# Kernel tuning notes

Hardware: AMD Instinct MI355X
Metric: run time of the kernel (lower is better)

Reference implementation:

```python
import math
import jax, jax.numpy as jnp
import numpy as np

D, H, NB, L, K = 45, 256, 6, 2, 8          # features, hidden, maf blocks, made hidden layers, spline bins
M = 3 * K - 1                               # params per feature (tails='linear')
TAIL = -math.log(1e-6)                      # tail_bound = -log(alpha)
MIN_BW = MIN_BH = MIN_D = 1e-3


def _masks():
    # nflows MADE sequential degrees (random_mask=False)
    d_in = np.arange(1, D + 1)
    d_h = (np.arange(H) % (D - 1)) + 1
    m0 = (d_h[:, None] >= d_in[None, :]).astype(np.float32)   # [H, D]
    mh = (d_h[:, None] >= d_h[None, :]).astype(np.float32)    # [H, H]
    d_out = np.repeat(d_in, M)                                 # nflows tile(): each degree repeated M times
    mf = (d_out[:, None] > d_h[None, :]).astype(np.float32)   # [D*M, H], strict for output layer
    return jnp.asarray(m0), jnp.asarray(mh), jnp.asarray(mf)


def _rq_spline(x, params):
    # x: [B, D]; params: [B, D, M]. unconstrained_rational_quadratic_spline, tails='linear'.
    uw = params[..., :K] / math.sqrt(H)        # nflows divides by sqrt(hidden_features)
    uh = params[..., K:2 * K] / math.sqrt(H)
    const = math.log(math.exp(1.0 - MIN_D) - 1.0)
    ud = jnp.pad(params[..., 2 * K:], ((0, 0), (0, 0), (1, 1)), constant_values=const)  # [B,D,K+1]
    inside = (x >= -TAIL) & (x <= TAIL)
    xc = jnp.clip(x, -TAIL, TAIL)

    def bin_edges(u, mn):
        p = jax.nn.softmax(u, -1)
        p = mn + (1.0 - mn * K) * p
        c = jnp.pad(jnp.cumsum(p, -1), ((0, 0), (0, 0), (1, 0)))
        c = 2.0 * TAIL * c - TAIL
        c = c.at[..., 0].set(-TAIL).at[..., -1].set(TAIL)
        return c, c[..., 1:] - c[..., :-1]

    cw, w = bin_edges(uw, MIN_BW)              # cumwidths [B,D,K+1], widths [B,D,K]
    ch, h = bin_edges(uh, MIN_BH)
    d = MIN_D + jax.nn.softplus(ud)            # derivatives [B,D,K+1]

    idx = jnp.clip(jnp.sum((xc[..., None] >= cw), -1) - 1, 0, K - 1)[..., None]
    g = lambda a: jnp.take_along_axis(a, idx, -1)[..., 0]
    icw, ibw, ich, ih = g(cw[..., :-1]), g(w), g(ch[..., :-1]), g(h)
    idelta = g(h / w)
    id0, id1 = g(d[..., :-1]), g(d[..., 1:])

    th = (xc - icw) / ibw
    th1 = th * (1.0 - th)
    den = idelta + (id0 + id1 - 2.0 * idelta) * th1
    y = ich + ih * (idelta * th * th + id0 * th1) / den
    lad = jnp.log(idelta * idelta * (id1 * th * th + 2.0 * idelta * th1 + id0 * (1.0 - th) ** 2)) - 2.0 * jnp.log(den)
    return jnp.where(inside, y, x), jnp.where(inside, lad, 0.0)


def setup_inputs() -> dict:
    key = jax.random.key(0)
    ks = jax.random.split(key, 10)
    B, s = 32768, 0.02
    return {
        "x": jax.random.normal(ks[0], (B, D), jnp.float32),
        "cond": jax.random.normal(ks[1], (B, 1), jnp.float32),
        "W0": jax.random.normal(ks[2], (NB, H, D), jnp.float32) * s,
        "b0": jax.random.normal(ks[3], (NB, H), jnp.float32) * s,
        "Wc": jax.random.normal(ks[4], (NB, H, 1), jnp.float32) * s,
        "bc": jax.random.normal(ks[5], (NB, H), jnp.float32) * s,
        "Wh": jax.random.normal(ks[6], (NB, L, H, H), jnp.float32) * s,
        "bh": jax.random.normal(ks[7], (NB, L, H), jnp.float32) * s,
        "Wf": jax.random.normal(ks[8], (NB, D * M, H), jnp.float32) * s,
        "bf": jax.random.normal(ks[9], (NB, D * M), jnp.float32) * s,
    }


def reference(x, cond, W0, b0, Wc, bc, Wh, bh, Wf, bf):
    m0, mh, mf = _masks()
    z = x
    ld = jnp.zeros(x.shape[0], x.dtype)
    for b in range(NB):  # CompositeTransform of NB MAF blocks
        hid = z @ (W0[b] * m0).T + b0[b] + cond @ Wc[b].T + bc[b]
        for l in range(L):  # MaskedFeedforwardBlock: linear -> ReLU (dropout=0, no BN)
            hid = jax.nn.relu(hid @ (Wh[b, l] * mh).T + bh[b, l])
        params = (hid @ (Wf[b] * mf).T + bf[b]).reshape(z.shape[0], D, M)
        z, lad = _rq_spline(z, params)
        ld = ld + lad.sum(-1)
    log_z = 0.5 * D * math.log(2.0 * math.pi)
    return -0.5 * jnp.sum(z * z, axis=1) - log_z + ld
```

## Files before the change

kernel.cpp:

```cpp
#include <hip/hip_runtime.h>


typedef __bf16 bf16;
typedef __bf16 bf16x8 __attribute__((ext_vector_type(8)));
typedef float  f32x16 __attribute__((ext_vector_type(16)));

#define TAILF  13.815510557964274f
#define TAIL2  27.631021115928548f
#define CMIN   0.027631021115928548f
#define LOGZ   41.352233994210265f

#define WS_W0M   0
#define WS_WHM   196608
#define WS_WFM   1769472
#define WS_BEFF  5210112
#define WS_BFP   5216256
#define WS_WCC   5243136
#define WS_BHP   5249280
#define WS_NEED  5261568

#define N_W0  (6*256*64)
#define N_WH  (6*2*256*256)
#define N_WF  (6*5*224*256)
#define N_PREP (N_W0 + N_WH + N_WF)

__device__ __forceinline__ int s_deg(int s) {
    return (s < 216) ? (s / 6) : (36 + (s - 216) / 5);
}
__device__ __forceinline__ int s_orig(int s) {
    int d, rk;
    if (s < 216) { d = s / 6; rk = s - d * 6; }
    else { int u = s - 216; d = 36 + u / 5; rk = u - (u / 5) * 5; }
    return d + 44 * rk;
}

__global__ void prep_all(const float* __restrict__ W0, const float* __restrict__ b0,
                         const float* __restrict__ Wc, const float* __restrict__ bc,
                         const float* __restrict__ Wh, const float* __restrict__ Wf,
                         const float* __restrict__ bfv, const float* __restrict__ bh,
                         bf16* __restrict__ W0m, bf16* __restrict__ Whm,
                         bf16* __restrict__ Wfm,
                         float* __restrict__ beff, float* __restrict__ bfp,
                         float* __restrict__ Wcc, float* __restrict__ bhp)
{
    int idx = blockIdx.x * 256 + threadIdx.x;
    if (idx < N_W0) {
        int j = idx & 7, lane = (idx >> 3) & 63, chunk = idx >> 9;
        int kt = chunk & 3, cg = (chunk >> 2) & 7, b = chunk >> 5;
        int col = cg * 32 + (lane & 31);
        int k   = kt * 16 + (lane >> 5) * 8 + j;
        int o   = s_orig(col);
        float v = 0.f;
        if (k < 45 && s_deg(col) >= k)
            v = W0[(b * 256 + o) * 45 + k];
        W0m[idx] = (bf16)v;
        if (k == 0) {
            beff[b * 256 + col] = b0[b * 256 + o] + bc[b * 256 + o];
            Wcc[b * 256 + col]  = Wc[b * 256 + o];
        }
    } else if (idx < N_W0 + N_WH) {
        int id = idx - N_W0;
        int j = id & 7, lane = (id >> 3) & 63, chunk = id >> 9;
        int kt = chunk & 15, cg = (chunk >> 4) & 7, bl = chunk >> 7;
        int col = cg * 32 + (lane & 31);
        int k   = kt * 16 + (lane >> 5) * 8 + j;
        int oc  = s_orig(col), ok = s_orig(k);
        float v = (s_deg(col) >= s_deg(k)) ? Wh[bl * 65536 + oc * 256 + ok] : 0.f;
        Whm[id] = (bf16)v;
        if (k == 0)
            bhp[bl * 256 + col] = bh[bl * 256 + oc];
    } else if (idx < N_PREP) {
        int id = idx - (N_W0 + N_WH);
        int j = id & 7, lane = (id >> 3) & 63, chunk = id >> 9;
        int kt = chunk & 15, t2 = chunk >> 4;
        int cg = t2 % 7, bg = t2 / 7;
        int b  = bg / 5, g = bg - 5 * b;
        int col = cg * 32 + (lane & 31);
        int k   = kt * 16 + (lane >> 5) * 8 + j;
        int ok  = s_orig(k);
        int f   = 9 * g + col / 23;
        int m   = col - (col / 23) * 23;
        bool valid = (col < 207);
        float v = 0.f;
        if (valid && (f > s_deg(k)))
            v = Wf[(b * 1035 + f * 23 + m) * 256 + ok];
        Wfm[id] = (bf16)v;
        if (k == 0)
            bfp[bg * 224 + col] = valid ? bfv[b * 1035 + f * 23 + m] : 0.f;
    }
}

#define SO_ZF    0
#define SO_ZB    11776
#define SO_HIDA  18944
#define SO_PBUF  52736
#define SO_COND  80528
#define SO_LD    80784
#define SMEM_BYTES 81040

#define PBF 1544

__constant__ unsigned char IN_NP[8]     = {1,1,1,1,1,1,2,2};
__constant__ unsigned char HID_NP[8]    = {2,3,3,5,6,6,8,8};
__constant__ unsigned char OUT_NP[5][7] = {
    {1,1,1,1,2,2,2},
    {2,3,3,3,3,4,4},
    {4,4,5,5,5,5,5},
    {6,6,6,6,7,7,7},
    {7,8,8,8,8,8,8}};

template<int MODE>
__device__ __forceinline__ void epi32(const f32x16& acc, int cg, int hf,
    const float* __restrict__ bias, const float* __restrict__ wcol,
    const float* condl, bf16* dst, int l31, int kh8)
{
    const int col = cg * 32 + l31;
    if (MODE == 2 && col >= 207) return;
    const float bv = bias[col];
    const int rb = (kh8 >> 1) + hf * 32;
    if (MODE == 2) {
        const int fl = col / 23, m = col - fl * 23;
        bf16* dp = dst + fl * PBF + m;
        #pragma unroll
        for (int r = 0; r < 16; ++r) {
            int row = (r & 3) + 8 * (r >> 2) + rb;
            dp[row * 24] = (bf16)(acc[r] + bv);
        }
    } else {
        const float wcv = (MODE == 0) ? wcol[col] : 0.f;
        #pragma unroll
        for (int r = 0; r < 16; ++r) {
            int row = (r & 3) + 8 * (r >> 2) + rb;
            float v = acc[r] + bv;
            if (MODE == 0) v += condl[row] * wcv;
            if (MODE == 1) v = fmaxf(v, 0.f);
            dst[row * 264 + col] = (bf16)v;
        }
    }
}

template<int KTFULL, int MODE>
__device__ __forceinline__ void gemm64(
    const bf16* Asrc, const int lda,
    const bf16* __restrict__ Wp,
    const float* __restrict__ bias, const float* __restrict__ wcol,
    const float* condl, bf16* dst,
    int cg, int np, int halfmask,
    int lane, bool preEpiSync)
{
    const int l31 = lane & 31;
    const int kh8 = (lane >> 5) * 8;
    const bf16* Bp  = Wp + (size_t)cg * (KTFULL * 512) + lane * 8;
    const bf16* Alo = Asrc + l31 * lda + kh8;
    const bf16* Ahi = Alo + 32 * lda;

    f32x16 acc0 = {}, acc1 = {};
    bf16x8 rA0, rA1, rB0, rB1, rC0, rC1;

#define LB(c)  (*reinterpret_cast<const bf16x8*>(Bp + (size_t)(c) * 512))
#define LAL(c) (*reinterpret_cast<const bf16x8*>(Alo + (c) * 16))
#define LAH(c) (*reinterpret_cast<const bf16x8*>(Ahi + (c) * 16))
#define CHUNK(breg, c) { \
    bf16x8 a0_ = LAL(c), a1_ = LAH(c); \
    acc0 = __builtin_amdgcn_mfma_f32_32x32x16_bf16(a0_, breg, acc0, 0, 0, 0); \
    acc1 = __builtin_amdgcn_mfma_f32_32x32x16_bf16(a1_, breg, acc1, 0, 0, 0); }
#define LP(r0, r1, p) { r0 = LB(2*(p)); r1 = LB(2*(p)+1); }
#define CP(r0, r1, p) { CHUNK(r0, 2*(p)) CHUNK(r1, 2*(p)+1) }

    LP(rA0, rA1, 0);
    if (np > 1) LP(rB0, rB1, 1);
    if (np > 2) LP(rC0, rC1, 2);

    int p = 0;
    #pragma unroll 1
    while (p + 3 < np) {
        CP(rA0, rA1, p);
        LP(rA0, rA1, p + 3);
        CP(rB0, rB1, p + 1);
        if (p + 4 < np) LP(rB0, rB1, p + 4);
        CP(rC0, rC1, p + 2);
        if (p + 5 < np) LP(rC0, rC1, p + 5);
        p += 3;
    }
    CP(rA0, rA1, p);
    if (np - p > 1) CP(rB0, rB1, p + 1);
    if (np - p > 2) CP(rC0, rC1, p + 2);

#undef LB
#undef LAL
#undef LAH
#undef CHUNK
#undef LP
#undef CP

    if (preEpiSync) __syncthreads();

    if (halfmask & 1) epi32<MODE>(acc0, cg, 0, bias, wcol, condl, dst, l31, kh8);
    if (halfmask & 2) epi32<MODE>(acc1, cg, 1, bias, wcol, condl, dst, l31, kh8);
    __syncthreads();
}

__device__ __forceinline__ void do_spline9(int fb, float* zf, bf16* zb,
                                           const bf16* pbuf, int t, float& lad_acc)
{
    #pragma unroll 1
    for (int task = t; task < 576; task += 512) {
        int fl = task >> 6, r = task & 63;
        const bf16* pp = pbuf + fl * PBF + r * 24;
        bf16x8 q0 = *reinterpret_cast<const bf16x8*>(pp);
        bf16x8 q1 = *reinterpret_cast<const bf16x8*>(pp + 8);
        bf16x8 q2 = *reinterpret_cast<const bf16x8*>(pp + 16);
        float P[23];
        #pragma unroll
        for (int m = 0; m < 8; ++m) P[m]      = (float)q0[m];
        #pragma unroll
        for (int m = 0; m < 8; ++m) P[8 + m]  = (float)q1[m];
        #pragma unroll
        for (int m = 0; m < 7; ++m) P[16 + m] = (float)q2[m];

        float xin = zf[r * 46 + fb + fl];
        float xc  = fminf(fmaxf(xin, -TAILF), TAILF);
        bool inside = (xin >= -TAILF) && (xin <= TAILF);

        float mw = P[0];
        #pragma unroll
        for (int i = 1; i < 8; ++i) mw = fmaxf(mw, P[i]);
        float ew[8], sw = 0.f;
        #pragma unroll
        for (int i = 0; i < 8; ++i) { ew[i] = __expf((P[i] - mw) * 0.0625f); sw += ew[i]; }
        float rws = TAIL2 * 0.992f / sw;
        float cw[9], wb[8];
        cw[0] = -TAILF;
        #pragma unroll
        for (int i = 0; i < 8; ++i) {
            wb[i] = fmaf(ew[i], rws, CMIN);
            cw[i + 1] = cw[i] + wb[i];
        }
        cw[8] = TAILF;
        wb[7] = TAILF - cw[7];

        float mh = P[8];
        #pragma unroll
        for (int i = 1; i < 8; ++i) mh = fmaxf(mh, P[8 + i]);
        float eh[8], sh = 0.f;
        #pragma unroll
        for (int i = 0; i < 8; ++i) { eh[i] = __expf((P[8 + i] - mh) * 0.0625f); sh += eh[i]; }
        float rhs = TAIL2 * 0.992f / sh;
        float ch[9], hb[8];
        ch[0] = -TAILF;
        #pragma unroll
        for (int i = 0; i < 8; ++i) {
            hb[i] = fmaf(eh[i], rhs, CMIN);
            ch[i + 1] = ch[i] + hb[i];
        }
        ch[8] = TAILF;
        hb[7] = TAILF - ch[7];

        float dd[9];
        dd[0] = 1.0f; dd[8] = 1.0f;
        #pragma unroll
        for (int i = 1; i < 8; ++i)
            dd[i] = 1e-3f + __logf(1.f + __expf(P[15 + i]));

        float icw = cw[0], ich = ch[0], ibw = wb[0], ibh = hb[0];
        float id0 = dd[0], id1 = dd[1];
        #pragma unroll
        for (int i = 1; i < 8; ++i) {
            bool ge = xc >= cw[i];
            icw = ge ? cw[i] : icw;  ich = ge ? ch[i] : ich;
            ibw = ge ? wb[i] : ibw;  ibh = ge ? hb[i] : ibh;
            id0 = ge ? dd[i] : id0;  id1 = ge ? dd[i + 1] : id1;
        }

        float th  = (xc - icw) / ibw;
        float th1 = th * (1.f - th);
        float dl  = ibh / ibw;
        float den = dl + (id0 + id1 - 2.f * dl) * th1;
        float yy  = ich + ibh * (dl * th * th + id0 * th1) / den;
        float num = dl * dl * (id1 * th * th + 2.f * dl * th1
                               + id0 * (1.f - th) * (1.f - th));
        float lad = __logf(num) - 2.f * __logf(den);

        if (inside) {
            zf[r * 46 + fb + fl] = yy;
            zb[r * 56 + fb + fl] = (bf16)yy;
        }
        lad_acc += inside ? lad : 0.f;
    }
}

__global__ __launch_bounds__(512, 2) void maf_main(
    const float* __restrict__ x, const float* __restrict__ cond,
    const bf16* __restrict__ W0m, const bf16* __restrict__ Whm,
    const bf16* __restrict__ Wfm,
    const float* __restrict__ beff, const float* __restrict__ bfp,
    const float* __restrict__ Wcc, const float* __restrict__ bhp,
    float* __restrict__ out, int B)
{
    extern __shared__ char smem[];
    float* zf    = (float*)(smem + SO_ZF);
    bf16*  zb    = (bf16*)(smem + SO_ZB);
    bf16*  hidA  = (bf16*)(smem + SO_HIDA);
    bf16*  pbuf  = (bf16*)(smem + SO_PBUF);
    float* condl = (float*)(smem + SO_COND);
    float* ldl   = (float*)(smem + SO_LD);

    const int t    = threadIdx.x;
    const int r0   = blockIdx.x * 64;
    const int w    = t >> 6;
    const int lane = t & 63;
    const int wu   = __builtin_amdgcn_readfirstlane(w);

    for (int i = t; i < 64 * 11; i += 512) {
        int r = i / 11, c = i - (i / 11) * 11;
        zb[r * 56 + 45 + c] = (bf16)0.f;
    }
    if (t < 8) hidA[t] = (bf16)0.f;
    for (int i = t; i < 64 * 45; i += 512) {
        int r = i / 45, f = i - (i / 45) * 45;
        float v = (r0 + r < B) ? x[(size_t)(r0 + r) * 45 + f] : 0.f;
        zf[r * 46 + f] = v;
        zb[r * 56 + f] = (bf16)v;
    }
    if (t < 64) {
        condl[t] = (r0 + t < B) ? cond[r0 + t] : 0.f;
        ldl[t]   = 0.f;
    }
    __syncthreads();

    float lad_acc = 0.f;

    const int inNp  = IN_NP[wu];
    const int hidNp = HID_NP[wu];
    const int ocg   = (wu <= 5) ? wu : 6;
    const int ohm   = (wu <= 5) ? 3 : ((wu == 6) ? 1 : 2);

    #pragma unroll 1
    for (int b = 0; b < 6; ++b) {
        gemm64<4, 0>(zb, 56, W0m + b * 16384,
                     beff + b * 256, Wcc + b * 256, condl,
                     hidA, wu, inNp, 3, lane, false);
        #pragma unroll 1
        for (int l = 0; l < 2; ++l)
            gemm64<16, 1>(hidA, 264, Whm + (b * 2 + l) * 65536,
                          bhp + (b * 2 + l) * 256, nullptr, condl,
                          hidA, wu, hidNp, 3, lane, true);
        #pragma unroll 1
        for (int g = 0; g < 5; ++g) {
            gemm64<16, 2>(hidA, 264, Wfm + (size_t)(b * 5 + g) * 57344,
                          bfp + (b * 5 + g) * 224, nullptr, condl,
                          pbuf, ocg, OUT_NP[g][ocg], ohm, lane, g > 0);
            do_spline9(g * 9, zf, zb, pbuf, t, lad_acc);
        }
        __syncthreads();
    }

    atomicAdd(&ldl[t & 63], lad_acc);
    __syncthreads();

    if (t < 64 && r0 + t < B) {
        float s = 0.f;
        #pragma unroll
        for (int f = 0; f < 45; ++f) { float v = zf[t * 46 + f]; s += v * v; }
        out[r0 + t] = -0.5f * s - LOGZ + ldl[t];
    }
}

extern "C" void kernel_launch(void* const* d_in, const int* in_sizes, int n_in,
                              void* d_out, int out_size, void* d_ws, size_t ws_size,
                              hipStream_t stream)
{
    const float* x    = (const float*)d_in[0];
    const float* cond = (const float*)d_in[1];
    const float* W0   = (const float*)d_in[2];
    const float* b0   = (const float*)d_in[3];
    const float* Wc   = (const float*)d_in[4];
    const float* bc   = (const float*)d_in[5];
    const float* Wh   = (const float*)d_in[6];
    const float* bh   = (const float*)d_in[7];
    const float* Wf   = (const float*)d_in[8];
    const float* bfv  = (const float*)d_in[9];
    float* out = (float*)d_out;

    const int B = in_sizes[0] / 45;
    if (ws_size < (size_t)WS_NEED) return;

    char* ws = (char*)d_ws;
    bf16*  W0m  = (bf16*)(ws + WS_W0M);
    bf16*  Whm  = (bf16*)(ws + WS_WHM);
    bf16*  Wfm  = (bf16*)(ws + WS_WFM);
    float* beff = (float*)(ws + WS_BEFF);
    float* bfp  = (float*)(ws + WS_BFP);
    float* Wcc  = (float*)(ws + WS_WCC);
    float* bhp  = (float*)(ws + WS_BHP);

    prep_all<<<(N_PREP + 255) / 256, 256, 0, stream>>>(
        W0, b0, Wc, bc, Wh, Wf, bfv, bh, W0m, Whm, Wfm, beff, bfp, Wcc, bhp);

    (void)hipFuncSetAttribute((const void*)maf_main,
                              hipFuncAttributeMaxDynamicSharedMemorySize,
                              SMEM_BYTES);

    const int nwg = (B + 63) / 64;
    maf_main<<<nwg, 512, SMEM_BYTES, stream>>>(
        x, cond, W0m, Whm, Wfm, beff, bfp, Wcc, bhp, out, B);
}
```

Baseline: 326.7 us.

## Halve rows per workgroup to 32 and double workgroup occupancy

Each workgroup now processes 32 batch rows instead of 64. Each wave issues one MFMA accumulator instead of two, so per-wave register use drops, and the shared-memory footprint is halved. Launch bounds go from 2 to 4 blocks per CU and twice as many workgroups launch. The aim is more parallelism and latency hiding, but each weight tile loaded from global memory is now reused over half as many rows, roughly doubling weight traffic. The spline stage now uses only 288 of 512 threads, and wave 7 sits idle in the output GEMM.

```diff
diff --git a/kernel.cpp b/kernel.cpp
--- a/kernel.cpp
+++ b/kernel.cpp
@@ -91,14 +91,14 @@
 }
 
 #define SO_ZF    0
-#define SO_ZB    11776
-#define SO_HIDA  18944
-#define SO_PBUF  52736
-#define SO_COND  80528
-#define SO_LD    80784
-#define SMEM_BYTES 81040
-
-#define PBF 1544
+#define SO_ZB    5888
+#define SO_HIDA  9472
+#define SO_PBUF  26368
+#define SO_COND  40336
+#define SO_LD    40464
+#define SMEM_BYTES 40592
+
+#define PBF 776
 
 __constant__ unsigned char IN_NP[8]     = {1,1,1,1,1,1,2,2};
 __constant__ unsigned char HID_NP[8]    = {2,3,3,5,6,6,8,8};
@@ -110,14 +110,14 @@
     {7,8,8,8,8,8,8}};
 
 template<int MODE>
-__device__ __forceinline__ void epi32(const f32x16& acc, int cg, int hf,
+__device__ __forceinline__ void epi32(const f32x16& acc, int cg,
     const float* __restrict__ bias, const float* __restrict__ wcol,
     const float* condl, bf16* dst, int l31, int kh8)
 {
     const int col = cg * 32 + l31;
     if (MODE == 2 && col >= 207) return;
     const float bv = bias[col];
-    const int rb = (kh8 >> 1) + hf * 32;
+    const int rb = kh8 >> 1;
     if (MODE == 2) {
         const int fl = col / 23, m = col - fl * 23;
         bf16* dp = dst + fl * PBF + m;
@@ -140,156 +140,151 @@
 }
 
 template<int KTFULL, int MODE>
-__device__ __forceinline__ void gemm64(
+__device__ __forceinline__ void gemm32r(
     const bf16* Asrc, const int lda,
     const bf16* __restrict__ Wp,
     const float* __restrict__ bias, const float* __restrict__ wcol,
     const float* condl, bf16* dst,
-    int cg, int np, int halfmask,
+    int cg, int np,
     int lane, bool preEpiSync)
 {
     const int l31 = lane & 31;
     const int kh8 = (lane >> 5) * 8;
-    const bf16* Bp  = Wp + (size_t)cg * (KTFULL * 512) + lane * 8;
-    const bf16* Alo = Asrc + l31 * lda + kh8;
-    const bf16* Ahi = Alo + 32 * lda;
-
-    f32x16 acc0 = {}, acc1 = {};
+    const bf16* Bp = Wp + (size_t)cg * (KTFULL * 512) + lane * 8;
+    const bf16* Ap = Asrc + l31 * lda + kh8;
+
+    f32x16 acc = {};
     bf16x8 rA0, rA1, rB0, rB1, rC0, rC1;
 
 #define LB(c)  (*reinterpret_cast<const bf16x8*>(Bp + (size_t)(c) * 512))
-#define LAL(c) (*reinterpret_cast<const bf16x8*>(Alo + (c) * 16))
-#define LAH(c) (*reinterpret_cast<const bf16x8*>(Ahi + (c) * 16))
+#define LA(c)  (*reinterpret_cast<const bf16x8*>(Ap + (c) * 16))
 #define CHUNK(breg, c) { \
-    bf16x8 a0_ = LAL(c), a1_ = LAH(c); \
-    acc0 = __builtin_amdgcn_mfma_f32_32x32x16_bf16(a0_, breg, acc0, 0, 0, 0); \
-    acc1 = __builtin_amdgcn_mfma_f32_32x32x16_bf16(a1_, breg, acc1, 0, 0, 0); }
+    bf16x8 a_ = LA(c); \
+    acc = __builtin_amdgcn_mfma_f32_32x32x16_bf16(a_, breg, acc, 0, 0, 0); }
 #define LP(r0, r1, p) { r0 = LB(2*(p)); r1 = LB(2*(p)+1); }
 #define CP(r0, r1, p) { CHUNK(r0, 2*(p)) CHUNK(r1, 2*(p)+1) }
 
-    LP(rA0, rA1, 0);
-    if (np > 1) LP(rB0, rB1, 1);
-    if (np > 2) LP(rC0, rC1, 2);
-
-    int p = 0;
-    #pragma unroll 1
-    while (p + 3 < np) {
+    if (np > 0) {
+        LP(rA0, rA1, 0);
+        if (np > 1) LP(rB0, rB1, 1);
+        if (np > 2) LP(rC0, rC1, 2);
+
+        int p = 0;
+        #pragma unroll 1
+        while (p + 3 < np) {
+            CP(rA0, rA1, p);
+            LP(rA0, rA1, p + 3);
+            CP(rB0, rB1, p + 1);
+            if (p + 4 < np) LP(rB0, rB1, p + 4);
+            CP(rC0, rC1, p + 2);
+            if (p + 5 < np) LP(rC0, rC1, p + 5);
+            p += 3;
+        }
         CP(rA0, rA1, p);
-        LP(rA0, rA1, p + 3);
-        CP(rB0, rB1, p + 1);
-        if (p + 4 < np) LP(rB0, rB1, p + 4);
-        CP(rC0, rC1, p + 2);
-        if (p + 5 < np) LP(rC0, rC1, p + 5);
-        p += 3;
-    }
-    CP(rA0, rA1, p);
-    if (np - p > 1) CP(rB0, rB1, p + 1);
-    if (np - p > 2) CP(rC0, rC1, p + 2);
+        if (np - p > 1) CP(rB0, rB1, p + 1);
+        if (np - p > 2) CP(rC0, rC1, p + 2);
+    }
 
 #undef LB
-#undef LAL
-#undef LAH
+#undef LA
 #undef CHUNK
 #undef LP
 #undef CP
 
     if (preEpiSync) __syncthreads();
 
-    if (halfmask & 1) epi32<MODE>(acc0, cg, 0, bias, wcol, condl, dst, l31, kh8);
-    if (halfmask & 2) epi32<MODE>(acc1, cg, 1, bias, wcol, condl, dst, l31, kh8);
+    if (np > 0) epi32<MODE>(acc, cg, bias, wcol, condl, dst, l31, kh8);
     __syncthreads();
 }
 
 __device__ __forceinline__ void do_spline9(int fb, float* zf, bf16* zb,
                                            const bf16* pbuf, int t, float& lad_acc)
 {
-    #pragma unroll 1
-    for (int task = t; task < 576; task += 512) {
-        int fl = task >> 6, r = task & 63;
-        const bf16* pp = pbuf + fl * PBF + r * 24;
-        bf16x8 q0 = *reinterpret_cast<const bf16x8*>(pp);
-        bf16x8 q1 = *reinterpret_cast<const bf16x8*>(pp + 8);
-        bf16x8 q2 = *reinterpret_cast<const bf16x8*>(pp + 16);
-        float P[23];
-        #pragma unroll
-        for (int m = 0; m < 8; ++m) P[m]      = (float)q0[m];
-        #pragma unroll
-        for (int m = 0; m < 8; ++m) P[8 + m]  = (float)q1[m];
-        #pragma unroll
-        for (int m = 0; m < 7; ++m) P[16 + m] = (float)q2[m];
-
-        float xin = zf[r * 46 + fb + fl];
-        float xc  = fminf(fmaxf(xin, -TAILF), TAILF);
-        bool inside = (xin >= -TAILF) && (xin <= TAILF);
-
-        float mw = P[0];
-        #pragma unroll
-        for (int i = 1; i < 8; ++i) mw = fmaxf(mw, P[i]);
-        float ew[8], sw = 0.f;
-        #pragma unroll
-        for (int i = 0; i < 8; ++i) { ew[i] = __expf((P[i] - mw) * 0.0625f); sw += ew[i]; }
-        float rws = TAIL2 * 0.992f / sw;
-        float cw[9], wb[8];
-        cw[0] = -TAILF;
-        #pragma unroll
-        for (int i = 0; i < 8; ++i) {
-            wb[i] = fmaf(ew[i], rws, CMIN);
-            cw[i + 1] = cw[i] + wb[i];
-        }
-        cw[8] = TAILF;
-        wb[7] = TAILF - cw[7];
-
-        float mh = P[8];
-        #pragma unroll
-        for (int i = 1; i < 8; ++i) mh = fmaxf(mh, P[8 + i]);
-        float eh[8], sh = 0.f;
-        #pragma unroll
-        for (int i = 0; i < 8; ++i) { eh[i] = __expf((P[8 + i] - mh) * 0.0625f); sh += eh[i]; }
-        float rhs = TAIL2 * 0.992f / sh;
-        float ch[9], hb[8];
-        ch[0] = -TAILF;
-        #pragma unroll
-        for (int i = 0; i < 8; ++i) {
-            hb[i] = fmaf(eh[i], rhs, CMIN);
-            ch[i + 1] = ch[i] + hb[i];
-        }
-        ch[8] = TAILF;
-        hb[7] = TAILF - ch[7];
-
-        float dd[9];
-        dd[0] = 1.0f; dd[8] = 1.0f;
-        #pragma unroll
-        for (int i = 1; i < 8; ++i)
-            dd[i] = 1e-3f + __logf(1.f + __expf(P[15 + i]));
-
-        float icw = cw[0], ich = ch[0], ibw = wb[0], ibh = hb[0];
-        float id0 = dd[0], id1 = dd[1];
-        #pragma unroll
-        for (int i = 1; i < 8; ++i) {
-            bool ge = xc >= cw[i];
-            icw = ge ? cw[i] : icw;  ich = ge ? ch[i] : ich;
-            ibw = ge ? wb[i] : ibw;  ibh = ge ? hb[i] : ibh;
-            id0 = ge ? dd[i] : id0;  id1 = ge ? dd[i + 1] : id1;
-        }
-
-        float th  = (xc - icw) / ibw;
-        float th1 = th * (1.f - th);
-        float dl  = ibh / ibw;
-        float den = dl + (id0 + id1 - 2.f * dl) * th1;
-        float yy  = ich + ibh * (dl * th * th + id0 * th1) / den;
-        float num = dl * dl * (id1 * th * th + 2.f * dl * th1
-                               + id0 * (1.f - th) * (1.f - th));
-        float lad = __logf(num) - 2.f * __logf(den);
-
-        if (inside) {
-            zf[r * 46 + fb + fl] = yy;
-            zb[r * 56 + fb + fl] = (bf16)yy;
-        }
-        lad_acc += inside ? lad : 0.f;
-    }
-}
-
-__global__ __launch_bounds__(512, 2) void maf_main(
+    if (t >= 288) return;
+    const int fl = t >> 5, r = t & 31;
+    const bf16* pp = pbuf + fl * PBF + r * 24;
+    bf16x8 q0 = *reinterpret_cast<const bf16x8*>(pp);
+    bf16x8 q1 = *reinterpret_cast<const bf16x8*>(pp + 8);
+    bf16x8 q2 = *reinterpret_cast<const bf16x8*>(pp + 16);
+    float P[23];
+    #pragma unroll
+    for (int m = 0; m < 8; ++m) P[m]      = (float)q0[m];
+    #pragma unroll
+    for (int m = 0; m < 8; ++m) P[8 + m]  = (float)q1[m];
+    #pragma unroll
+    for (int m = 0; m < 7; ++m) P[16 + m] = (float)q2[m];
+
+    float xin = zf[r * 46 + fb + fl];
+    float xc  = fminf(fmaxf(xin, -TAILF), TAILF);
+    bool inside = (xin >= -TAILF) && (xin <= TAILF);
+
+    float mw = P[0];
+    #pragma unroll
+    for (int i = 1; i < 8; ++i) mw = fmaxf(mw, P[i]);
+    float ew[8], sw = 0.f;
+    #pragma unroll
+    for (int i = 0; i < 8; ++i) { ew[i] = __expf((P[i] - mw) * 0.0625f); sw += ew[i]; }
+    float rws = TAIL2 * 0.992f / sw;
+    float cw[9], wb[8];
+    cw[0] = -TAILF;
+    #pragma unroll
+    for (int i = 0; i < 8; ++i) {
+        wb[i] = fmaf(ew[i], rws, CMIN);
+        cw[i + 1] = cw[i] + wb[i];
+    }
+    cw[8] = TAILF;
+    wb[7] = TAILF - cw[7];
+
+    float mh = P[8];
+    #pragma unroll
+    for (int i = 1; i < 8; ++i) mh = fmaxf(mh, P[8 + i]);
+    float eh[8], sh = 0.f;
+    #pragma unroll
+    for (int i = 0; i < 8; ++i) { eh[i] = __expf((P[8 + i] - mh) * 0.0625f); sh += eh[i]; }
+    float rhs = TAIL2 * 0.992f / sh;
+    float ch[9], hb[8];
+    ch[0] = -TAILF;
+    #pragma unroll
+    for (int i = 0; i < 8; ++i) {
+        hb[i] = fmaf(eh[i], rhs, CMIN);
+        ch[i + 1] = ch[i] + hb[i];
+    }
+    ch[8] = TAILF;
+    hb[7] = TAILF - ch[7];
+
+    float dd[9];
+    dd[0] = 1.0f; dd[8] = 1.0f;
+    #pragma unroll
+    for (int i = 1; i < 8; ++i)
+        dd[i] = 1e-3f + __logf(1.f + __expf(P[15 + i]));
+
+    float icw = cw[0], ich = ch[0], ibw = wb[0], ibh = hb[0];
+    float id0 = dd[0], id1 = dd[1];
+    #pragma unroll
+    for (int i = 1; i < 8; ++i) {
+        bool ge = xc >= cw[i];
+        icw = ge ? cw[i] : icw;  ich = ge ? ch[i] : ich;
+        ibw = ge ? wb[i] : ibw;  ibh = ge ? hb[i] : ibh;
+        id0 = ge ? dd[i] : id0;  id1 = ge ? dd[i + 1] : id1;
+    }
+
+    float th  = (xc - icw) / ibw;
+    float th1 = th * (1.f - th);
+    float dl  = ibh / ibw;
+    float den = dl + (id0 + id1 - 2.f * dl) * th1;
+    float yy  = ich + ibh * (dl * th * th + id0 * th1) / den;
+    float num = dl * dl * (id1 * th * th + 2.f * dl * th1
+                           + id0 * (1.f - th) * (1.f - th));
+    float lad = __logf(num) - 2.f * __logf(den);
+
+    if (inside) {
+        zf[r * 46 + fb + fl] = yy;
+        zb[r * 56 + fb + fl] = (bf16)yy;
+    }
+    lad_acc += inside ? lad : 0.f;
+}
+
+__global__ __launch_bounds__(512, 4) void maf_main(
     const float* __restrict__ x, const float* __restrict__ cond,
     const bf16* __restrict__ W0m, const bf16* __restrict__ Whm,
     const bf16* __restrict__ Wfm,
@@ -306,23 +301,23 @@
     float* ldl   = (float*)(smem + SO_LD);
 
     const int t    = threadIdx.x;
-    const int r0   = blockIdx.x * 64;
+    const int r0   = blockIdx.x * 32;
     const int w    = t >> 6;
     const int lane = t & 63;
     const int wu   = __builtin_amdgcn_readfirstlane(w);
 
-    for (int i = t; i < 64 * 11; i += 512) {
+    for (int i = t; i < 32 * 11; i += 512) {
         int r = i / 11, c = i - (i / 11) * 11;
         zb[r * 56 + 45 + c] = (bf16)0.f;
     }
     if (t < 8) hidA[t] = (bf16)0.f;
-    for (int i = t; i < 64 * 45; i += 512) {
+    for (int i = t; i < 32 * 45; i += 512) {
         int r = i / 45, f = i - (i / 45) * 45;
         float v = (r0 + r < B) ? x[(size_t)(r0 + r) * 45 + f] : 0.f;
         zf[r * 46 + f] = v;
         zb[r * 56 + f] = (bf16)v;
     }
-    if (t < 64) {
+    if (t < 32) {
         condl[t] = (r0 + t < B) ? cond[r0 + t] : 0.f;
         ldl[t]   = 0.f;
     }
@@ -332,33 +327,33 @@
 
     const int inNp  = IN_NP[wu];
     const int hidNp = HID_NP[wu];
-    const int ocg   = (wu <= 5) ? wu : 6;
-    const int ohm   = (wu <= 5) ? 3 : ((wu == 6) ? 1 : 2);
+    const int oNpOk = (wu < 7);
 
     #pragma unroll 1
     for (int b = 0; b < 6; ++b) {
-        gemm64<4, 0>(zb, 56, W0m + b * 16384,
-                     beff + b * 256, Wcc + b * 256, condl,
-                     hidA, wu, inNp, 3, lane, false);
+        gemm32r<4, 0>(zb, 56, W0m + b * 16384,
+                      beff + b * 256, Wcc + b * 256, condl,
+                      hidA, wu, inNp, lane, false);
         #pragma unroll 1
         for (int l = 0; l < 2; ++l)
-            gemm64<16, 1>(hidA, 264, Whm + (b * 2 + l) * 65536,
-                          bhp + (b * 2 + l) * 256, nullptr, condl,
-                          hidA, wu, hidNp, 3, lane, true);
+            gemm32r<16, 1>(hidA, 264, Whm + (b * 2 + l) * 65536,
+                           bhp + (b * 2 + l) * 256, nullptr, condl,
+                           hidA, wu, hidNp, lane, true);
         #pragma unroll 1
         for (int g = 0; g < 5; ++g) {
-            gemm64<16, 2>(hidA, 264, Wfm + (size_t)(b * 5 + g) * 57344,
-                          bfp + (b * 5 + g) * 224, nullptr, condl,
-                          pbuf, ocg, OUT_NP[g][ocg], ohm, lane, g > 0);
+            gemm32r<16, 2>(hidA, 264, Wfm + (size_t)(b * 5 + g) * 57344,
+                           bfp + (b * 5 + g) * 224, nullptr, condl,
+                           pbuf, oNpOk ? wu : 0, oNpOk ? OUT_NP[g][wu] : 0,
+                           lane, g > 0);
             do_spline9(g * 9, zf, zb, pbuf, t, lad_acc);
         }
         __syncthreads();
     }
 
-    atomicAdd(&ldl[t & 63], lad_acc);
+    atomicAdd(&ldl[t & 31], lad_acc);
     __syncthreads();
 
-    if (t < 64 && r0 + t < B) {
+    if (t < 32 && r0 + t < B) {
         float s = 0.f;
         #pragma unroll
         for (int f = 0; f < 45; ++f) { float v = zf[t * 46 + f]; s += v * v; }
@@ -401,7 +396,7 @@
                               hipFuncAttributeMaxDynamicSharedMemorySize,
                               SMEM_BYTES);
 
-    const int nwg = (B + 63) / 64;
+    const int nwg = (B + 31) / 32;
     maf_main<<<nwg, 512, SMEM_BYTES, stream>>>(
         x, cond, W0m, Whm, Wfm, beff, bfp, Wcc, bhp, out, B);
 }
```

Result: slower. 382.2 us (+17.0%).

## Overlap spline evaluation with next output-GEMM group via per-wave work split

Applied to the files above, without the earlier changes.

Restructures the final-layer loop so that, for groups 1-4, each wave first evaluates its assigned spline features for the previous group and then issues the next output GEMM, using per-wave start/count tables. Waves with less GEMM work (wave 7) take more spline features, balancing load and letting spline math overlap MFMA work across waves. Each group now needs one barrier before the epilogue writes pbuf and one after, and the final group's spline runs after the loop. The spline work is now assigned per feature-wave, 64 rows by lane, instead of a strided 576-task loop, which depends on the hand-built tables being correct.

```diff
diff --git a/kernel.cpp b/kernel.cpp
--- a/kernel.cpp
+++ b/kernel.cpp
@@ -109,6 +109,19 @@
     {6,6,6,6,7,7,7},
     {7,8,8,8,8,8,8}};
 
+__constant__ unsigned char SPL_START[5][8] = {
+    {0,2,3,4,5,6,0,7},
+    {0,1,2,3,4,5,0,6},
+    {0,1,2,3,4,5,0,6},
+    {0,2,3,4,5,0,0,6},
+    {0,2,3,4,5,6,7,8}};
+__constant__ unsigned char SPL_CNT[5][8] = {
+    {2,1,1,1,1,1,0,2},
+    {1,1,1,1,1,1,0,3},
+    {1,1,1,1,1,1,0,3},
+    {2,1,1,1,1,0,0,3},
+    {2,1,1,1,1,1,1,1}};
+
 template<int MODE>
 __device__ __forceinline__ void epi32(const f32x16& acc, int cg, int hf,
     const float* __restrict__ bias, const float* __restrict__ wcol,
@@ -139,14 +152,10 @@
     }
 }
 
-template<int KTFULL, int MODE>
-__device__ __forceinline__ void gemm64(
-    const bf16* Asrc, const int lda,
-    const bf16* __restrict__ Wp,
-    const float* __restrict__ bias, const float* __restrict__ wcol,
-    const float* condl, bf16* dst,
-    int cg, int np, int halfmask,
-    int lane, bool preEpiSync)
+template<int KTFULL>
+__device__ __forceinline__ void gemm_compute(
+    const bf16* Asrc, const int lda, const bf16* __restrict__ Wp,
+    int cg, int np, int lane, f32x16& acc0, f32x16& acc1)
 {
     const int l31 = lane & 31;
     const int kh8 = (lane >> 5) * 8;
@@ -154,7 +163,8 @@
     const bf16* Alo = Asrc + l31 * lda + kh8;
     const bf16* Ahi = Alo + 32 * lda;
 
-    f32x16 acc0 = {}, acc1 = {};
+    acc0 = (f32x16){};
+    acc1 = (f32x16){};
     bf16x8 rA0, rA1, rB0, rB1, rC0, rC1;
 
 #define LB(c)  (*reinterpret_cast<const bf16x8*>(Bp + (size_t)(c) * 512))
@@ -192,101 +202,99 @@
 #undef CHUNK
 #undef LP
 #undef CP
-
-    if (preEpiSync) __syncthreads();
-
-    if (halfmask & 1) epi32<MODE>(acc0, cg, 0, bias, wcol, condl, dst, l31, kh8);
-    if (halfmask & 2) epi32<MODE>(acc1, cg, 1, bias, wcol, condl, dst, l31, kh8);
-    __syncthreads();
-}
-
-__device__ __forceinline__ void do_spline9(int fb, float* zf, bf16* zb,
-                                           const bf16* pbuf, int t, float& lad_acc)
+}
+
+__device__ __forceinline__ void spline_task(int fb, int fl, int r,
+    float* zf, bf16* zb, const bf16* pbuf, float& lad_acc)
+{
+    const bf16* pp = pbuf + fl * PBF + r * 24;
+    bf16x8 q0 = *reinterpret_cast<const bf16x8*>(pp);
+    bf16x8 q1 = *reinterpret_cast<const bf16x8*>(pp + 8);
+    bf16x8 q2 = *reinterpret_cast<const bf16x8*>(pp + 16);
+    float P[23];
+    #pragma unroll
+    for (int m = 0; m < 8; ++m) P[m]      = (float)q0[m];
+    #pragma unroll
+    for (int m = 0; m < 8; ++m) P[8 + m]  = (float)q1[m];
+    #pragma unroll
+    for (int m = 0; m < 7; ++m) P[16 + m] = (float)q2[m];
+
+    float xin = zf[r * 46 + fb + fl];
+    float xc  = fminf(fmaxf(xin, -TAILF), TAILF);
+    bool inside = (xin >= -TAILF) && (xin <= TAILF);
+
+    float mw = P[0];
+    #pragma unroll
+    for (int i = 1; i < 8; ++i) mw = fmaxf(mw, P[i]);
+    float ew[8], sw = 0.f;
+    #pragma unroll
+    for (int i = 0; i < 8; ++i) { ew[i] = __expf((P[i] - mw) * 0.0625f); sw += ew[i]; }
+    float rws = TAIL2 * 0.992f / sw;
+    float cw[9], wb[8];
+    cw[0] = -TAILF;
+    #pragma unroll
+    for (int i = 0; i < 8; ++i) {
+        wb[i] = fmaf(ew[i], rws, CMIN);
+        cw[i + 1] = cw[i] + wb[i];
+    }
+    cw[8] = TAILF;
+    wb[7] = TAILF - cw[7];
+
+    float mh = P[8];
+    #pragma unroll
+    for (int i = 1; i < 8; ++i) mh = fmaxf(mh, P[8 + i]);
+    float eh[8], sh = 0.f;
+    #pragma unroll
+    for (int i = 0; i < 8; ++i) { eh[i] = __expf((P[8 + i] - mh) * 0.0625f); sh += eh[i]; }
+    float rhs = TAIL2 * 0.992f / sh;
+    float ch[9], hb[8];
+    ch[0] = -TAILF;
+    #pragma unroll
+    for (int i = 0; i < 8; ++i) {
+        hb[i] = fmaf(eh[i], rhs, CMIN);
+        ch[i + 1] = ch[i] + hb[i];
+    }
+    ch[8] = TAILF;
+    hb[7] = TAILF - ch[7];
+
+    float dd[9];
+    dd[0] = 1.0f; dd[8] = 1.0f;
+    #pragma unroll
+    for (int i = 1; i < 8; ++i)
+        dd[i] = 1e-3f + __logf(1.f + __expf(P[15 + i]));
+
+    float icw = cw[0], ich = ch[0], ibw = wb[0], ibh = hb[0];
+    float id0 = dd[0], id1 = dd[1];
+    #pragma unroll
+    for (int i = 1; i < 8; ++i) {
+        bool ge = xc >= cw[i];
+        icw = ge ? cw[i] : icw;  ich = ge ? ch[i] : ich;
+        ibw = ge ? wb[i] : ibw;  ibh = ge ? hb[i] : ibh;
+        id0 = ge ? dd[i] : id0;  id1 = ge ? dd[i + 1] : id1;
+    }
+
+    float th  = (xc - icw) / ibw;
+    float th1 = th * (1.f - th);
+    float dl  = ibh / ibw;
+    float den = dl + (id0 + id1 - 2.f * dl) * th1;
+    float yy  = ich + ibh * (dl * th * th + id0 * th1) / den;
+    float num = dl * dl * (id1 * th * th + 2.f * dl * th1
+                           + id0 * (1.f - th) * (1.f - th));
+    float lad = __logf(num) - 2.f * __logf(den);
+
+    if (inside) {
+        zf[r * 46 + fb + fl] = yy;
+        zb[r * 56 + fb + fl] = (bf16)yy;
+    }
+    lad_acc += inside ? lad : 0.f;
+}
+
+__device__ __forceinline__ void spline_units(int fb, int start, int cnt,
+    float* zf, bf16* zb, const bf16* pbuf, int lane, float& lad_acc)
 {
     #pragma unroll 1
-    for (int task = t; task < 576; task += 512) {
-        int fl = task >> 6, r = task & 63;
-        const bf16* pp = pbuf + fl * PBF + r * 24;
-        bf16x8 q0 = *reinterpret_cast<const bf16x8*>(pp);
-        bf16x8 q1 = *reinterpret_cast<const bf16x8*>(pp + 8);
-        bf16x8 q2 = *reinterpret_cast<const bf16x8*>(pp + 16);
-        float P[23];
-        #pragma unroll
-        for (int m = 0; m < 8; ++m) P[m]      = (float)q0[m];
-        #pragma unroll
-        for (int m = 0; m < 8; ++m) P[8 + m]  = (float)q1[m];
-        #pragma unroll
-        for (int m = 0; m < 7; ++m) P[16 + m] = (float)q2[m];
-
-        float xin = zf[r * 46 + fb + fl];
-        float xc  = fminf(fmaxf(xin, -TAILF), TAILF);
-        bool inside = (xin >= -TAILF) && (xin <= TAILF);
-
-        float mw = P[0];
-        #pragma unroll
-        for (int i = 1; i < 8; ++i) mw = fmaxf(mw, P[i]);
-        float ew[8], sw = 0.f;
-        #pragma unroll
-        for (int i = 0; i < 8; ++i) { ew[i] = __expf((P[i] - mw) * 0.0625f); sw += ew[i]; }
-        float rws = TAIL2 * 0.992f / sw;
-        float cw[9], wb[8];
-        cw[0] = -TAILF;
-        #pragma unroll
-        for (int i = 0; i < 8; ++i) {
-            wb[i] = fmaf(ew[i], rws, CMIN);
-            cw[i + 1] = cw[i] + wb[i];
-        }
-        cw[8] = TAILF;
-        wb[7] = TAILF - cw[7];
-
-        float mh = P[8];
-        #pragma unroll
-        for (int i = 1; i < 8; ++i) mh = fmaxf(mh, P[8 + i]);
-        float eh[8], sh = 0.f;
-        #pragma unroll
-        for (int i = 0; i < 8; ++i) { eh[i] = __expf((P[8 + i] - mh) * 0.0625f); sh += eh[i]; }
-        float rhs = TAIL2 * 0.992f / sh;
-        float ch[9], hb[8];
-        ch[0] = -TAILF;
-        #pragma unroll
-        for (int i = 0; i < 8; ++i) {
-            hb[i] = fmaf(eh[i], rhs, CMIN);
-            ch[i + 1] = ch[i] + hb[i];
-        }
-        ch[8] = TAILF;
-        hb[7] = TAILF - ch[7];
-
-        float dd[9];
-        dd[0] = 1.0f; dd[8] = 1.0f;
-        #pragma unroll
-        for (int i = 1; i < 8; ++i)
-            dd[i] = 1e-3f + __logf(1.f + __expf(P[15 + i]));
-
-        float icw = cw[0], ich = ch[0], ibw = wb[0], ibh = hb[0];
-        float id0 = dd[0], id1 = dd[1];
-        #pragma unroll
-        for (int i = 1; i < 8; ++i) {
-            bool ge = xc >= cw[i];
-            icw = ge ? cw[i] : icw;  ich = ge ? ch[i] : ich;
-            ibw = ge ? wb[i] : ibw;  ibh = ge ? hb[i] : ibh;
-            id0 = ge ? dd[i] : id0;  id1 = ge ? dd[i + 1] : id1;
-        }
-
-        float th  = (xc - icw) / ibw;
-        float th1 = th * (1.f - th);
-        float dl  = ibh / ibw;
-        float den = dl + (id0 + id1 - 2.f * dl) * th1;
-        float yy  = ich + ibh * (dl * th * th + id0 * th1) / den;
-        float num = dl * dl * (id1 * th * th + 2.f * dl * th1
-                               + id0 * (1.f - th) * (1.f - th));
-        float lad = __logf(num) - 2.f * __logf(den);
-
-        if (inside) {
-            zf[r * 46 + fb + fl] = yy;
-            zb[r * 56 + fb + fl] = (bf16)yy;
-        }
-        lad_acc += inside ? lad : 0.f;
-    }
+    for (int k = 0; k < cnt; ++k)
+        spline_task(fb, start + k, lane, zf, zb, pbuf, lad_acc);
 }
 
 __global__ __launch_bounds__(512, 2) void maf_main(
@@ -310,6 +318,8 @@
     const int w    = t >> 6;
     const int lane = t & 63;
     const int wu   = __builtin_amdgcn_readfirstlane(w);
+    const int l31  = lane & 31;
+    const int kh8  = (lane >> 5) * 8;
 
     for (int i = t; i < 64 * 11; i += 512) {
         int r = i / 11, c = i - (i / 11) * 11;
@@ -332,26 +342,51 @@
 
     const int inNp  = IN_NP[wu];
     const int hidNp = HID_NP[wu];
-    const int ocg   = (wu <= 5) ? wu : 6;
-    const int ohm   = (wu <= 5) ? 3 : ((wu == 6) ? 1 : 2);
+    const int ocg0  = (wu <= 5) ? wu : 6;
 
     #pragma unroll 1
     for (int b = 0; b < 6; ++b) {
-        gemm64<4, 0>(zb, 56, W0m + b * 16384,
-                     beff + b * 256, Wcc + b * 256, condl,
-                     hidA, wu, inNp, 3, lane, false);
+        f32x16 a0, a1;
+        gemm_compute<4>(zb, 56, W0m + b * 16384, wu, inNp, lane, a0, a1);
+        epi32<0>(a0, wu, 0, beff + b * 256, Wcc + b * 256, condl, hidA, l31, kh8);
+        epi32<0>(a1, wu, 1, beff + b * 256, Wcc + b * 256, condl, hidA, l31, kh8);
+        __syncthreads();
         #pragma unroll 1
-        for (int l = 0; l < 2; ++l)
-            gemm64<16, 1>(hidA, 264, Whm + (b * 2 + l) * 65536,
-                          bhp + (b * 2 + l) * 256, nullptr, condl,
-                          hidA, wu, hidNp, 3, lane, true);
+        for (int l = 0; l < 2; ++l) {
+            gemm_compute<16>(hidA, 264, Whm + (b * 2 + l) * 65536,
+                             wu, hidNp, lane, a0, a1);
+            __syncthreads();
+            epi32<1>(a0, wu, 0, bhp + (b * 2 + l) * 256, nullptr, condl, hidA, l31, kh8);
+            epi32<1>(a1, wu, 1, bhp + (b * 2 + l) * 256, nullptr, condl, hidA, l31, kh8);
+            __syncthreads();
+        }
+        gemm_compute<16>(hidA, 264, Wfm + (size_t)(b * 5) * 57344,
+                         ocg0, OUT_NP[0][ocg0], lane, a0, a1);
+        if (wu <= 5) {
+            epi32<2>(a0, wu, 0, bfp + (b * 5) * 224, nullptr, condl, pbuf, l31, kh8);
+            epi32<2>(a1, wu, 1, bfp + (b * 5) * 224, nullptr, condl, pbuf, l31, kh8);
+        } else if (wu == 6) {
+            epi32<2>(a0, 6, 0, bfp + (b * 5) * 224, nullptr, condl, pbuf, l31, kh8);
+        } else {
+            epi32<2>(a1, 6, 1, bfp + (b * 5) * 224, nullptr, condl, pbuf, l31, kh8);
+        }
+        __syncthreads();
         #pragma unroll 1
-        for (int g = 0; g < 5; ++g) {
-            gemm64<16, 2>(hidA, 264, Wfm + (size_t)(b * 5 + g) * 57344,
-                          bfp + (b * 5 + g) * 224, nullptr, condl,
-                          pbuf, ocg, OUT_NP[g][ocg], ohm, lane, g > 0);
-            do_spline9(g * 9, zf, zb, pbuf, t, lad_acc);
-        }
+        for (int g = 1; g < 5; ++g) {
+            spline_units((g - 1) * 9, SPL_START[g - 1][wu], SPL_CNT[g - 1][wu],
+                         zf, zb, pbuf, lane, lad_acc);
+            if (wu < 7)
+                gemm_compute<16>(hidA, 264, Wfm + (size_t)(b * 5 + g) * 57344,
+                                 wu, OUT_NP[g][wu], lane, a0, a1);
+            __syncthreads();
+            if (wu < 7) {
+                epi32<2>(a0, wu, 0, bfp + (b * 5 + g) * 224, nullptr, condl, pbuf, l31, kh8);
+                epi32<2>(a1, wu, 1, bfp + (b * 5 + g) * 224, nullptr, condl, pbuf, l31, kh8);
+            }
+            __syncthreads();
+        }
+        spline_units(36, SPL_START[4][wu], SPL_CNT[4][wu],
+                     zf, zb, pbuf, lane, lad_acc);
         __syncthreads();
     }
 
```

After: 417.5 us. +27.8%, slower.
